# Kernel optimization log

Hardware: AMD Instinct MI355X
Metric: run time of the kernel (lower is better)

Reference implementation:

```python
import jax, jax.numpy as jnp
import numpy as np

TEMPERATURE = 0.1
BASE_TEMPERATURE = 1.0
LAMBDA_PROTOTYPE = 1.0
EPS = 1e-12  # F.normalize eps

N, C, D, P = 65536, 128, 512, 128


def setup_inputs() -> dict:
    key = jax.random.key(0)
    k1, k2, k3, k4, k5 = jax.random.split(key, 5)
    return {
        "outputs": jax.random.normal(k1, (N, C), dtype=jnp.float32),
        "targets": jax.random.normal(k2, (N, C), dtype=jnp.float32),
        "backbone_features": jax.random.normal(k3, (N, D), dtype=jnp.float32),
        "prototype_features": jax.random.normal(k4, (P, D), dtype=jnp.float32),
        "prototype_labels": jax.random.randint(k5, (N, P), 0, 2, dtype=jnp.int32),
        "prototype_weights": jnp.ones((P,), dtype=jnp.float32),
    }


def reference(outputs, targets, backbone_features, prototype_features,
              prototype_labels, prototype_weights):
    # L2-normalize backbone features along feature dim (F.normalize, dim=1)
    norm = jnp.maximum(jnp.linalg.norm(backbone_features, axis=1, keepdims=True), EPS)
    bf = backbone_features / norm  # (N, D)

    n = outputs.reshape(-1, outputs.shape[-1]).shape[0]

    # Batched version of the per-sample loop: one GEMM for all samples.
    logits = jnp.einsum('nd,pd->np', bf, prototype_features) / TEMPERATURE  # (N, P)
    # Per-sample max subtraction for stability (detached in torch)
    logits = logits - jax.lax.stop_gradient(jnp.max(logits, axis=1, keepdims=True))

    mask = prototype_labels.astype(logits.dtype) * prototype_weights  # (N, P)
    exp_logits = jnp.exp(logits) * (1.0 - mask)
    log_prob = logits - jnp.log(jnp.sum(exp_logits, axis=1, keepdims=True))  # (N, P)
    mean_log_prob_pos = jnp.sum(mask * log_prob, axis=1)  # (N,)

    ctr_loss = -(TEMPERATURE / BASE_TEMPERATURE) * mean_log_prob_pos
    loss = jnp.sum(ctr_loss) / n
    return LAMBDA_PROTOTYPE * loss
```

## Files before the change

kernel.cpp:

```cpp
#include <hip/hip_runtime.h>
#include <hip/hip_bf16.h>
#include <math.h>

typedef __bf16 bf16x8 __attribute__((ext_vector_type(8)));
typedef __bf16 bf16x4 __attribute__((ext_vector_type(4)));
typedef float  f32x4  __attribute__((ext_vector_type(4)));

#define D_DIM 512
#define P_DIM 128
#define MB    128
#define BK    64
#define LDA   72
#define TEMP  0.1f

__global__ __launch_bounds__(256, 2)
void mrc_fused(const float* __restrict__ bfeat,
               const float* __restrict__ protos,
               const int*   __restrict__ labels,
               const float* __restrict__ weights,
               float*       __restrict__ out,
               int nrows)
{
    __shared__ __bf16 sA[MB * LDA];
    __shared__ __bf16 sB[P_DIM * LDA];
    __shared__ float  sScale[MB];
    __shared__ float  sRed[4];

    const int t    = threadIdx.x;
    const int lane = t & 63;
    const int wave = t >> 6;
    const int rgrp = t >> 4;
    const int cidx = t & 15;
    const int q    = lane >> 4;
    const int cl   = lane & 15;

    const long long R0 = (long long)blockIdx.x * MB;

    float wcol[8];
#pragma unroll
    for (int ct = 0; ct < 8; ++ct) wcol[ct] = weights[ct * 16 + cl];

    float ss[8];
#pragma unroll
    for (int i = 0; i < 8; ++i) ss[i] = 0.f;

    f32x4 acc[2][8];
#pragma unroll
    for (int mt = 0; mt < 2; ++mt)
#pragma unroll
        for (int ct = 0; ct < 8; ++ct) acc[mt][ct] = (f32x4){0.f, 0.f, 0.f, 0.f};

    for (int kc = 0; kc < D_DIM / BK; ++kc) {
        const int kbase = kc * BK;

#pragma unroll
        for (int i = 0; i < 8; ++i) {
            const int row = i * 16 + rgrp;
            const float4 v = *(const float4*)(bfeat + (R0 + row) * D_DIM + kbase + cidx * 4);
            ss[i] += v.x * v.x + v.y * v.y + v.z * v.z + v.w * v.w;
            bf16x4 b;
            b[0] = (__bf16)v.x; b[1] = (__bf16)v.y; b[2] = (__bf16)v.z; b[3] = (__bf16)v.w;
            *(bf16x4*)&sA[row * LDA + cidx * 4] = b;
        }
#pragma unroll
        for (int i = 0; i < 8; ++i) {
            const int row = i * 16 + rgrp;
            const float4 v = *(const float4*)(protos + row * D_DIM + kbase + cidx * 4);
            bf16x4 b;
            b[0] = (__bf16)v.x; b[1] = (__bf16)v.y; b[2] = (__bf16)v.z; b[3] = (__bf16)v.w;
            *(bf16x4*)&sB[row * LDA + cidx * 4] = b;
        }
        __syncthreads();

#pragma unroll
        for (int ks = 0; ks < 2; ++ks) {
            const int k0 = ks * 32;
            bf16x8 af[2];
#pragma unroll
            for (int mt = 0; mt < 2; ++mt) {
                const int r = wave * 32 + mt * 16 + cl;
                af[mt] = *(const bf16x8*)&sA[r * LDA + k0 + q * 8];
            }
#pragma unroll
            for (int ct = 0; ct < 8; ++ct) {
                const int n = ct * 16 + cl;
                const bf16x8 bfr = *(const bf16x8*)&sB[n * LDA + k0 + q * 8];
#pragma unroll
                for (int mt = 0; mt < 2; ++mt)
                    acc[mt][ct] = __builtin_amdgcn_mfma_f32_16x16x32_bf16(af[mt], bfr, acc[mt][ct], 0, 0, 0);
            }
        }
        __syncthreads();
    }

#pragma unroll
    for (int i = 0; i < 8; ++i) {
        float s = ss[i];
        s += __shfl_xor(s, 1, 16);
        s += __shfl_xor(s, 2, 16);
        s += __shfl_xor(s, 4, 16);
        s += __shfl_xor(s, 8, 16);
        if (cl == 0) {
            const int row = i * 16 + rgrp;
            const float nrm = fmaxf(sqrtf(s), 1e-12f);
            sScale[row] = 1.0f / (nrm * TEMP);
        }
    }
    __syncthreads();

    float pos_acc = 0.f;
#pragma unroll
    for (int mt = 0; mt < 2; ++mt) {
#pragma unroll
        for (int reg = 0; reg < 4; ++reg) {
            const int rl = wave * 32 + mt * 16 + q * 4 + reg;
            const float scale = sScale[rl];
            float lg[8];
            float m = -3.4e38f;
#pragma unroll
            for (int ct = 0; ct < 8; ++ct) {
                lg[ct] = acc[mt][ct][reg] * scale;
                m = fmaxf(m, lg[ct]);
            }
            m = fmaxf(m, __shfl_xor(m, 1, 16));
            m = fmaxf(m, __shfl_xor(m, 2, 16));
            m = fmaxf(m, __shfl_xor(m, 4, 16));
            m = fmaxf(m, __shfl_xor(m, 8, 16));

            const int* lrow = labels + (R0 + rl) * (long long)P_DIM;
            float s = 0.f, p = 0.f, msum = 0.f;
#pragma unroll
            for (int ct = 0; ct < 8; ++ct) {
                const float mask = (float)lrow[ct * 16 + cl] * wcol[ct];
                const float z = lg[ct] - m;
                s    += __expf(z) * (1.0f - mask);
                p    += mask * z;
                msum += mask;
            }
            s += __shfl_xor(s, 1, 16);
            s += __shfl_xor(s, 2, 16);
            s += __shfl_xor(s, 4, 16);
            s += __shfl_xor(s, 8, 16);
            pos_acc += p - logf(s) * msum;
        }
    }

    pos_acc += __shfl_xor(pos_acc, 1);
    pos_acc += __shfl_xor(pos_acc, 2);
    pos_acc += __shfl_xor(pos_acc, 4);
    pos_acc += __shfl_xor(pos_acc, 8);
    pos_acc += __shfl_xor(pos_acc, 16);
    pos_acc += __shfl_xor(pos_acc, 32);
    if (lane == 0) sRed[wave] = pos_acc;
    __syncthreads();
    if (t == 0) {
        const float total = sRed[0] + sRed[1] + sRed[2] + sRed[3];
        atomicAdd(out, total * (-TEMP / (float)nrows));
    }
}

extern "C" void kernel_launch(void* const* d_in, const int* in_sizes, int n_in,
                              void* d_out, int out_size, void* d_ws, size_t ws_size,
                              hipStream_t stream) {
    const float* bfeat   = (const float*)d_in[2];
    const float* protos  = (const float*)d_in[3];
    const int*   labels  = (const int*)d_in[4];
    const float* weights = (const float*)d_in[5];
    float* out = (float*)d_out;

    const int nrows = in_sizes[2] / D_DIM;

    hipMemsetAsync(d_out, 0, sizeof(float) * out_size, stream);
    const int nblocks = nrows / MB;
    mrc_fused<<<nblocks, 256, 0, stream>>>(bfeat, protos, labels, weights, out, nrows);
}
```

Before: 284.7 us.

## Stage full prototype matrix in LDS once and load A fragments directly into registers

```diff
diff --git a/kernel.cpp b/kernel.cpp
--- a/kernel.cpp
+++ b/kernel.cpp
@@ -2,18 +2,18 @@
 #include <hip/hip_bf16.h>
 #include <math.h>
 
-typedef __bf16 bf16x8 __attribute__((ext_vector_type(8)));
-typedef __bf16 bf16x4 __attribute__((ext_vector_type(4)));
-typedef float  f32x4  __attribute__((ext_vector_type(4)));
+typedef __bf16 bf16x8v __attribute__((ext_vector_type(8)));
+typedef __bf16 bf16x4v __attribute__((ext_vector_type(4)));
+typedef float  f32x4   __attribute__((ext_vector_type(4)));
 
 #define D_DIM 512
 #define P_DIM 128
-#define MB    128
-#define BK    64
-#define LDA   72
+#define LDB   520
 #define TEMP  0.1f
+#define ROWS_PER_BLOCK 256
+#define THREADS 1024
 
-__global__ __launch_bounds__(256, 2)
+__global__ __launch_bounds__(THREADS, 4)
 void mrc_fused(const float* __restrict__ bfeat,
                const float* __restrict__ protos,
                const int*   __restrict__ labels,
@@ -21,128 +21,98 @@
                float*       __restrict__ out,
                int nrows)
 {
-    __shared__ __bf16 sA[MB * LDA];
-    __shared__ __bf16 sB[P_DIM * LDA];
-    __shared__ float  sScale[MB];
-    __shared__ float  sRed[4];
+    __shared__ __bf16 sB[P_DIM * LDB];
+    __shared__ float  sRed[16];
 
     const int t    = threadIdx.x;
     const int lane = t & 63;
     const int wave = t >> 6;
-    const int rgrp = t >> 4;
-    const int cidx = t & 15;
     const int q    = lane >> 4;
     const int cl   = lane & 15;
 
-    const long long R0 = (long long)blockIdx.x * MB;
+#pragma unroll
+    for (int i = 0; i < 16; ++i) {
+        const int f   = i * THREADS + t;
+        const int row = f >> 7;
+        const int c4  = f & 127;
+        const float4 v = *(const float4*)(protos + row * D_DIM + c4 * 4);
+        bf16x4v b;
+        b[0] = (__bf16)v.x; b[1] = (__bf16)v.y; b[2] = (__bf16)v.z; b[3] = (__bf16)v.w;
+        *(bf16x4v*)&sB[row * LDB + c4 * 4] = b;
+    }
+    __syncthreads();
+
+    const long long r0 = (long long)blockIdx.x * ROWS_PER_BLOCK + wave * 16;
+    const float* arow = bfeat + (r0 + cl) * (long long)D_DIM + q * 8;
 
     float wcol[8];
 #pragma unroll
     for (int ct = 0; ct < 8; ++ct) wcol[ct] = weights[ct * 16 + cl];
 
-    float ss[8];
+    f32x4 acc[8];
 #pragma unroll
-    for (int i = 0; i < 8; ++i) ss[i] = 0.f;
+    for (int ct = 0; ct < 8; ++ct) acc[ct] = (f32x4){0.f, 0.f, 0.f, 0.f};
 
-    f32x4 acc[2][8];
+    float ss = 0.f;
+    float4 p0 = *(const float4*)(arow);
+    float4 p1 = *(const float4*)(arow + 4);
+
+#pragma unroll 4
+    for (int ks = 0; ks < 16; ++ks) {
+        const float4 c0 = p0, c1 = p1;
+        if (ks < 15) {
+            p0 = *(const float4*)(arow + (ks + 1) * 32);
+            p1 = *(const float4*)(arow + (ks + 1) * 32 + 4);
+        }
+        ss += c0.x*c0.x + c0.y*c0.y + c0.z*c0.z + c0.w*c0.w
+            + c1.x*c1.x + c1.y*c1.y + c1.z*c1.z + c1.w*c1.w;
+        bf16x8v af;
+        af[0]=(__bf16)c0.x; af[1]=(__bf16)c0.y; af[2]=(__bf16)c0.z; af[3]=(__bf16)c0.w;
+        af[4]=(__bf16)c1.x; af[5]=(__bf16)c1.y; af[6]=(__bf16)c1.z; af[7]=(__bf16)c1.w;
+        const int k0 = ks * 32 + q * 8;
 #pragma unroll
-    for (int mt = 0; mt < 2; ++mt)
-#pragma unroll
-        for (int ct = 0; ct < 8; ++ct) acc[mt][ct] = (f32x4){0.f, 0.f, 0.f, 0.f};
-
-    for (int kc = 0; kc < D_DIM / BK; ++kc) {
-        const int kbase = kc * BK;
-
-#pragma unroll
-        for (int i = 0; i < 8; ++i) {
-            const int row = i * 16 + rgrp;
-            const float4 v = *(const float4*)(bfeat + (R0 + row) * D_DIM + kbase + cidx * 4);
-            ss[i] += v.x * v.x + v.y * v.y + v.z * v.z + v.w * v.w;
-            bf16x4 b;
-            b[0] = (__bf16)v.x; b[1] = (__bf16)v.y; b[2] = (__bf16)v.z; b[3] = (__bf16)v.w;
-            *(bf16x4*)&sA[row * LDA + cidx * 4] = b;
+        for (int ct = 0; ct < 8; ++ct) {
+            const bf16x8v bfr = *(const bf16x8v*)&sB[(ct * 16 + cl) * LDB + k0];
+            acc[ct] = __builtin_amdgcn_mfma_f32_16x16x32_bf16(af, bfr, acc[ct], 0, 0, 0);
         }
-#pragma unroll
-        for (int i = 0; i < 8; ++i) {
-            const int row = i * 16 + rgrp;
-            const float4 v = *(const float4*)(protos + row * D_DIM + kbase + cidx * 4);
-            bf16x4 b;
-            b[0] = (__bf16)v.x; b[1] = (__bf16)v.y; b[2] = (__bf16)v.z; b[3] = (__bf16)v.w;
-            *(bf16x4*)&sB[row * LDA + cidx * 4] = b;
-        }
-        __syncthreads();
-
-#pragma unroll
-        for (int ks = 0; ks < 2; ++ks) {
-            const int k0 = ks * 32;
-            bf16x8 af[2];
-#pragma unroll
-            for (int mt = 0; mt < 2; ++mt) {
-                const int r = wave * 32 + mt * 16 + cl;
-                af[mt] = *(const bf16x8*)&sA[r * LDA + k0 + q * 8];
-            }
-#pragma unroll
-            for (int ct = 0; ct < 8; ++ct) {
-                const int n = ct * 16 + cl;
-                const bf16x8 bfr = *(const bf16x8*)&sB[n * LDA + k0 + q * 8];
-#pragma unroll
-                for (int mt = 0; mt < 2; ++mt)
-                    acc[mt][ct] = __builtin_amdgcn_mfma_f32_16x16x32_bf16(af[mt], bfr, acc[mt][ct], 0, 0, 0);
-            }
-        }
-        __syncthreads();
     }
 
+    ss += __shfl_xor(ss, 16);
+    ss += __shfl_xor(ss, 32);
+    const float scale = 1.0f / (fmaxf(sqrtf(ss), 1e-12f) * TEMP);
+
+    float pos_acc = 0.f;
 #pragma unroll
-    for (int i = 0; i < 8; ++i) {
-        float s = ss[i];
+    for (int reg = 0; reg < 4; ++reg) {
+        const int rl = q * 4 + reg;
+        const float rscale = __shfl(scale, rl, 16);
+        float lg[8];
+        float m = -3.4e38f;
+#pragma unroll
+        for (int ct = 0; ct < 8; ++ct) {
+            lg[ct] = acc[ct][reg] * rscale;
+            m = fmaxf(m, lg[ct]);
+        }
+        m = fmaxf(m, __shfl_xor(m, 1, 16));
+        m = fmaxf(m, __shfl_xor(m, 2, 16));
+        m = fmaxf(m, __shfl_xor(m, 4, 16));
+        m = fmaxf(m, __shfl_xor(m, 8, 16));
+
+        const int* lrow = labels + (r0 + rl) * (long long)P_DIM;
+        float s = 0.f, p = 0.f, msum = 0.f;
+#pragma unroll
+        for (int ct = 0; ct < 8; ++ct) {
+            const float mask = (float)lrow[ct * 16 + cl] * wcol[ct];
+            const float z = lg[ct] - m;
+            s    += __expf(z) * (1.0f - mask);
+            p    += mask * z;
+            msum += mask;
+        }
         s += __shfl_xor(s, 1, 16);
         s += __shfl_xor(s, 2, 16);
         s += __shfl_xor(s, 4, 16);
         s += __shfl_xor(s, 8, 16);
-        if (cl == 0) {
-            const int row = i * 16 + rgrp;
-            const float nrm = fmaxf(sqrtf(s), 1e-12f);
-            sScale[row] = 1.0f / (nrm * TEMP);
-        }
-    }
-    __syncthreads();
-
-    float pos_acc = 0.f;
-#pragma unroll
-    for (int mt = 0; mt < 2; ++mt) {
-#pragma unroll
-        for (int reg = 0; reg < 4; ++reg) {
-            const int rl = wave * 32 + mt * 16 + q * 4 + reg;
-            const float scale = sScale[rl];
-            float lg[8];
-            float m = -3.4e38f;
-#pragma unroll
-            for (int ct = 0; ct < 8; ++ct) {
-                lg[ct] = acc[mt][ct][reg] * scale;
-                m = fmaxf(m, lg[ct]);
-            }
-            m = fmaxf(m, __shfl_xor(m, 1, 16));
-            m = fmaxf(m, __shfl_xor(m, 2, 16));
-            m = fmaxf(m, __shfl_xor(m, 4, 16));
-            m = fmaxf(m, __shfl_xor(m, 8, 16));
-
-            const int* lrow = labels + (R0 + rl) * (long long)P_DIM;
-            float s = 0.f, p = 0.f, msum = 0.f;
-#pragma unroll
-            for (int ct = 0; ct < 8; ++ct) {
-                const float mask = (float)lrow[ct * 16 + cl] * wcol[ct];
-                const float z = lg[ct] - m;
-                s    += __expf(z) * (1.0f - mask);
-                p    += mask * z;
-                msum += mask;
-            }
-            s += __shfl_xor(s, 1, 16);
-            s += __shfl_xor(s, 2, 16);
-            s += __shfl_xor(s, 4, 16);
-            s += __shfl_xor(s, 8, 16);
-            pos_acc += p - logf(s) * msum;
-        }
+        pos_acc += p - logf(s) * msum;
     }
 
     pos_acc += __shfl_xor(pos_acc, 1);
@@ -154,7 +124,9 @@
     if (lane == 0) sRed[wave] = pos_acc;
     __syncthreads();
     if (t == 0) {
-        const float total = sRed[0] + sRed[1] + sRed[2] + sRed[3];
+        float total = 0.f;
+#pragma unroll
+        for (int w = 0; w < 16; ++w) total += sRed[w];
         atomicAdd(out, total * (-TEMP / (float)nrows));
     }
 }
@@ -171,6 +143,6 @@
     const int nrows = in_sizes[2] / D_DIM;
 
     hipMemsetAsync(d_out, 0, sizeof(float) * out_size, stream);
-    const int nblocks = nrows / MB;
-    mrc_fused<<<nblocks, 256, 0, stream>>>(bfeat, protos, labels, weights, out, nrows);
+    const int nblocks = nrows / ROWS_PER_BLOCK;
+    mrc_fused<<<nblocks, THREADS, 0, stream>>>(bfeat, protos, labels, weights, out, nrows);
 }
```

Result: faster. 257.5 us (-9.5%).
